# Performance work log

Hardware: AMD Instinct MI355X
Metric: run time of the kernel (lower is better)

Reference implementation:

```python
import jax, jax.numpy as jnp
import numpy as np

EPS = 1e-5

def _layer_norm_last(x):
    # F.layer_norm over the last dim, no affine
    m = jnp.mean(x, axis=-1, keepdims=True)
    v = jnp.var(x, axis=-1, keepdims=True)
    return (x - m) * jax.lax.rsqrt(v + EPS)

def setup_inputs() -> dict:
    key = jax.random.key(0)
    ks = jax.random.split(key, 4)
    N, C, H, W = 8, 512, 32, 32
    G = 8
    x = jax.random.normal(ks[0], (N, C, H, W), dtype=jnp.float32)
    w_qkv = jax.random.normal(ks[1], (3 * C, C), dtype=jnp.float32) * 0.02
    relative = jax.random.normal(ks[2], (3, 2 * C - 1), dtype=jnp.float32)
    bn_w = jnp.ones((3 * G,), dtype=jnp.float32)
    bn_b = jnp.zeros((3 * G,), dtype=jnp.float32)
    return {
        "x": x, "w_qkv": w_qkv, "relative": relative,
        "bn_w": bn_w, "bn_b": bn_b,
        "f_qr": jnp.float32(0.1), "f_kr": jnp.float32(0.1),
        "f_sv": jnp.float32(1.0), "f_sve": jnp.float32(0.1),
        "gamma": jnp.full((1,), 0.5, dtype=jnp.float32),
    }

def reference(x, w_qkv, relative, bn_w, bn_b, f_qr, f_kr, f_sv, f_sve, gamma):
    N, C, H, W = x.shape
    HW = H * W
    G = bn_w.shape[0] // 3          # groups
    gp = HW // G                    # group_planes

    # qkv transform (1x1 conv == matmul over channels) + layernorm over spatial
    x1 = x.reshape(N, C, HW)
    x1 = jnp.einsum('oc,bci->boi', w_qkv, x1)          # (N, 3C, HW)
    x1 = _layer_norm_last(x1)

    qkv = x1.reshape(N, G, 3 * C, gp)                  # row-major, matches torch
    q = qkv[:, :, :C]                                  # (N, G, C, gp)
    k = qkv[:, :, C:2 * C]
    v = qkv[:, :, 2 * C:]

    # relative position embeddings gathered to (3, C, C)
    qi = jnp.arange(C)[None, :]
    ki = jnp.arange(C)[:, None]
    rel_idx = (ki - qi + C - 1).reshape(-1)            # (C*C,) int
    emb = relative[:, rel_idx].reshape(3, C, C)
    qE, kE, vE = emb[0], emb[1], emb[2]

    # 'bgci,icj->bgcj' with emb repeated along i collapses to sum over i then outer
    qr = jnp.einsum('bgci,cj->bgcj', q, qE) * f_qr     # (N, G, C, C)
    kr = jnp.swapaxes(jnp.einsum('bgci,cj->bgcj', k, kE), 2, 3) * f_kr
    qk = jnp.einsum('bgci,bgji->bgcj', q, k)           # (N, G, C, C)

    ss = jnp.concatenate([qk, qr, kr], axis=1)         # (N, 3G, C, C)
    # BatchNorm2d (training mode: batch stats over N, C, C axes)
    mu = jnp.mean(ss, axis=(0, 2, 3), keepdims=True)
    var = jnp.var(ss, axis=(0, 2, 3), keepdims=True)
    ss = (ss - mu) * jax.lax.rsqrt(var + EPS)
    ss = ss * bn_w.reshape(1, -1, 1, 1) + bn_b.reshape(1, -1, 1, 1)

    ss = ss.reshape(N, 3, G, C, C).sum(axis=1)         # (N, G, C, C)
    sim = jax.nn.softmax(ss, axis=3)

    sv = jnp.einsum('bgci,bgij->bgjc', sim, v) * f_sv  # (N, G, gp, C)
    # 'bgci,jci->bgjc' with vE repeated along j -> same value for every j
    sve = jnp.einsum('bgci,ci->bgc', sim, vE) * f_sve  # (N, G, C)
    sve = jnp.broadcast_to(sve[:, :, None, :], sv.shape)

    so = jnp.concatenate([sv, sve], axis=-1).reshape(N, HW * 2, C)
    so = jnp.swapaxes(_layer_norm_last(jnp.swapaxes(so, 1, 2)), 1, 2)
    out = so.reshape(N, G, gp, 2, C).sum(axis=-2).reshape(N, C, H, W)
    return gamma.reshape(()) * out + x
```

## Files before the change

### kernel.cpp

```cpp
#include <hip/hip_runtime.h>
#include <math.h>

#define DEV_INLINE __device__ __forceinline__

typedef short bf16x8 __attribute__((ext_vector_type(8)));
typedef float f32x4  __attribute__((ext_vector_type(4)));


DEV_INLINE float bf2f(short h){
  union { unsigned u; float f; } x; x.u = ((unsigned)(unsigned short)h) << 16; return x.f;
}
DEV_INLINE short f2bf(float f){
  union { float f; unsigned u; } x; x.f = f;
  unsigned r = x.u + 0x7FFF + ((x.u >> 16) & 1);
  return (short)(r >> 16);
}

template<bool MAXOP>
DEV_INLINE float block_reduce_f(float v){
  __shared__ float tmp[4];
  const int lane = threadIdx.x & 63, w = threadIdx.x >> 6;
  #pragma unroll
  for (int off = 32; off; off >>= 1){
    float o = __shfl_down(v, off);
    v = MAXOP ? fmaxf(v, o) : (v + o);
  }
  __syncthreads();
  if (lane == 0) tmp[w] = v;
  __syncthreads();
  return MAXOP ? fmaxf(fmaxf(tmp[0], tmp[1]), fmaxf(tmp[2], tmp[3]))
               : (tmp[0] + tmp[1] + tmp[2] + tmp[3]);
}

DEV_INLINE double block_reduce_d(double v){
  __shared__ double tmp[4];
  const int lane = threadIdx.x & 63, w = threadIdx.x >> 6;
  #pragma unroll
  for (int off = 32; off; off >>= 1) v += __shfl_down(v, off);
  __syncthreads();
  if (lane == 0) tmp[w] = v;
  __syncthreads();
  return tmp[0] + tmp[1] + tmp[2] + tmp[3];
}


DEV_INLINE void stage_tile(const short* __restrict__ g, int ldk, char* lds_region, int t){
  #pragma unroll
  for (int r = 0; r < 2; ++r){
    int o   = t * 16 + r * 4096;
    int row = o >> 6, wb = o & 63;
    int swb = wb ^ (((row >> 1) & 3) << 4);
    const short* src = g + (size_t)row * ldk + (swb >> 1);
    char* dst = lds_region + ((t >> 6) << 10) + (r << 12);
    __builtin_amdgcn_global_load_lds((const __attribute__((address_space(1))) void*)src,
                                     (__attribute__((address_space(3))) void*)dst, 16, 0, 0);
  }
}

DEV_INLINE bf16x8 read_frag(const char* base, int row, int kgrp){
  int off = row * 64 + ((kgrp ^ ((row >> 1) & 3)) << 4);
  return *(const bf16x8*)(base + off);
}

template<int KTILES>
DEV_INLINE void mfma_loop(const short* __restrict__ A, int ldA,
                          const short* __restrict__ B, int ldB,
                          char* ldsA, char* ldsB, int t, f32x4 acc[4][4]){
  const int l = t & 63, w = t >> 6;
  const int wr = (w >> 1) * 64, wc = (w & 1) * 64;
  for (int kt = 0; kt < KTILES; ++kt){
    stage_tile(A + kt * 32, ldA, ldsA, t);
    stage_tile(B + kt * 32, ldB, ldsB, t);
    __syncthreads();
    bf16x8 af[4], bfr[4];
    #pragma unroll
    for (int m = 0; m < 4; ++m) af[m]  = read_frag(ldsA, wr + m * 16 + (l & 15), l >> 4);
    #pragma unroll
    for (int n = 0; n < 4; ++n) bfr[n] = read_frag(ldsB, wc + n * 16 + (l & 15), l >> 4);
    #pragma unroll
    for (int m = 0; m < 4; ++m)
      #pragma unroll
      for (int n = 0; n < 4; ++n)
        acc[m][n] = __builtin_amdgcn_mfma_f32_16x16x32_bf16(af[m], bfr[n], acc[m][n], 0, 0, 0);
    __syncthreads();
  }
}

__global__ __launch_bounds__(256) void k_prep(const float* __restrict__ X, short* __restrict__ Xt,
                                              const float* __restrict__ W, short* __restrict__ Wbf,
                                              double* __restrict__ stats, float* __restrict__ S12){
  __shared__ short s[64][72];
  const int bid = blockIdx.x;
  const int t = threadIdx.x;
  if (bid < 1024){
    const int it = bid & 15, kt = (bid >> 4) & 7, b = bid >> 7;
    const int rl = t >> 2, cs = (t & 3) * 16;
    const float* src = X + ((size_t)b * 512 + kt * 64 + rl) * 1024 + it * 64 + cs;
    #pragma unroll
    for (int e = 0; e < 16; e += 4){
      float4 v = *(const float4*)(src + e);
      s[rl][cs + e + 0] = f2bf(v.x); s[rl][cs + e + 1] = f2bf(v.y);
      s[rl][cs + e + 2] = f2bf(v.z); s[rl][cs + e + 3] = f2bf(v.w);
    }
    __syncthreads();
    bf16x8 a0, a1;
    #pragma unroll
    for (int e = 0; e < 8; ++e){ a0[e] = s[cs + e][rl]; a1[e] = s[cs + 8 + e][rl]; }
    short* dst = Xt + ((size_t)b * 1024 + it * 64 + rl) * 512 + kt * 64 + cs;
    *(bf16x8*)dst = a0;
    *(bf16x8*)(dst + 8) = a1;
  } else {
    const int gi = (bid - 1024) * 256 + t;
    if (gi < 48) stats[gi] = 0.0;
    if (gi < 8192) S12[gi] = 0.f;
    const int i = gi * 4;
    float4 v = *(const float4*)(W + i);
    short4 o; o.x = f2bf(v.x); o.y = f2bf(v.y); o.z = f2bf(v.z); o.w = f2bf(v.w);
    *(short4*)(Wbf + i) = o;
  }
}

__global__ __launch_bounds__(256) void k_vt(const short* __restrict__ Ybf, short* __restrict__ Vt){
  const int bg = blockIdx.z, iit = blockIdx.y, jt = blockIdx.x;
  const int b = bg >> 3, g = bg & 7;
  const short* V = Ybf + (size_t)(b * 1536 + g * 192 + 128) * 1024;
  __shared__ short s[64][72];
  const int t = threadIdx.x;
  const int rl = t >> 2, cs = (t & 3) * 16;
  const short* src = V + (size_t)(iit * 64 + rl) * 128 + jt * 64 + cs;
  *(bf16x8*)&s[rl][cs]     = *(const bf16x8*)src;
  *(bf16x8*)&s[rl][cs + 8] = *(const bf16x8*)(src + 8);
  __syncthreads();
  bf16x8 a0, a1;
  #pragma unroll
  for (int e = 0; e < 8; ++e){ a0[e] = s[cs + e][rl]; a1[e] = s[cs + 8 + e][rl]; }
  short* dst = Vt + ((size_t)bg * 128 + jt * 64 + rl) * 512 + iit * 64 + cs;
  *(bf16x8*)dst = a0;
  *(bf16x8*)(dst + 8) = a1;
}

__global__ __launch_bounds__(256) void k_gemm1(const short* __restrict__ Wbf,
                                               const short* __restrict__ Xt,
                                               short* __restrict__ Ybf){
  const int b = blockIdx.z, mt = blockIdx.y, nt = blockIdx.x;
  __shared__ char lds[16384];
  const int t = threadIdx.x;
  f32x4 acc[4][4];
  #pragma unroll
  for (int m = 0; m < 4; ++m)
    #pragma unroll
    for (int n = 0; n < 4; ++n) acc[m][n] = {0.f, 0.f, 0.f, 0.f};
  const short* A = Wbf + (size_t)mt * 128 * 512;
  const short* B = Xt + (size_t)b * 1024 * 512 + (size_t)nt * 128 * 512;
  mfma_loop<16>(A, 512, B, 512, lds, lds + 8192, t, acc);
  const int l = t & 63, w = t >> 6, wr = (w >> 1) * 64, wc = (w & 1) * 64;
  short* out = Ybf + (size_t)b * 1536 * 1024 + (size_t)(mt * 128 + wr) * 1024 + nt * 128 + wc;
  #pragma unroll
  for (int m = 0; m < 4; ++m)
    #pragma unroll
    for (int n = 0; n < 4; ++n)
      #pragma unroll
      for (int j = 0; j < 4; ++j)
        out[(size_t)(m * 16 + (l >> 4) * 4 + j) * 1024 + n * 16 + (l & 15)] = f2bf(acc[m][n][j]);
}

__global__ __launch_bounds__(256) void k_ln(short* __restrict__ Ybf,
                                            float* __restrict__ QS, float* __restrict__ KS){
  const int row = blockIdx.x * 4 + (threadIdx.x >> 6);
  const int l = threadIdx.x & 63;
  short* p = Ybf + (size_t)row * 1024 + l * 16;
  bf16x8 v0 = *(const bf16x8*)p;
  bf16x8 v1 = *(const bf16x8*)(p + 8);
  float f[16];
  #pragma unroll
  for (int e = 0; e < 8; ++e){ f[e] = bf2f(v0[e]); f[8 + e] = bf2f(v1[e]); }
  float s1 = 0.f, s2 = 0.f;
  #pragma unroll
  for (int e = 0; e < 16; ++e){ s1 += f[e]; s2 += f[e] * f[e]; }
  #pragma unroll
  for (int off = 32; off; off >>= 1){ s1 += __shfl_xor(s1, off); s2 += __shfl_xor(s2, off); }
  float mean = s1 * (1.f / 1024.f);
  float r = rsqrtf(s2 * (1.f / 1024.f) - mean * mean + 1e-5f);
  float cs = 0.f;
  #pragma unroll
  for (int e = 0; e < 16; ++e){ f[e] = (f[e] - mean) * r; cs += f[e]; }
  bf16x8 o0, o1;
  #pragma unroll
  for (int e = 0; e < 8; ++e){ o0[e] = f2bf(f[e]); o1[e] = f2bf(f[8 + e]); }
  *(bf16x8*)p = o0;
  *(bf16x8*)(p + 8) = o1;
  cs += __shfl_xor(cs, 1); cs += __shfl_xor(cs, 2); cs += __shfl_xor(cs, 4);
  const int o = row % 1536, ol = o % 192;
  if ((l & 7) == 0 && ol < 128){
    const int b = row / 1536, g = o / 192;
    const int c = (ol & 63) * 8 + (l >> 3);
    const int idx = (b * 8 + g) * 512 + c;
    if (ol < 64) QS[idx] = cs; else KS[idx] = cs;
  }
}

__global__ __launch_bounds__(256) void k_qk(const short* __restrict__ Ybf,
                                            short* __restrict__ QKbf,
                                            double* __restrict__ stats){
  const int bg = blockIdx.z, mt = blockIdx.y, nt = blockIdx.x;
  const int b = bg >> 3, g = bg & 7;
  __shared__ char lds[16384];
  const int t = threadIdx.x;
  f32x4 acc[4][4];
  #pragma unroll
  for (int m = 0; m < 4; ++m)
    #pragma unroll
    for (int n = 0; n < 4; ++n) acc[m][n] = {0.f, 0.f, 0.f, 0.f};
  const short* q  = Ybf + (size_t)(b * 1536 + g * 192) * 1024;
  const short* kp = q + 65536;
  mfma_loop<4>(q + (size_t)mt * 128 * 128, 128, kp + (size_t)nt * 128 * 128, 128,
               lds, lds + 8192, t, acc);
  const int l = t & 63, w = t >> 6, wr = (w >> 1) * 64, wc = (w & 1) * 64;
  short* out = QKbf + (size_t)bg * 512 * 512 + (size_t)(mt * 128 + wr) * 512 + nt * 128 + wc;
  float s1 = 0.f, s2 = 0.f;
  #pragma unroll
  for (int m = 0; m < 4; ++m)
    #pragma unroll
    for (int n = 0; n < 4; ++n)
      #pragma unroll
      for (int j = 0; j < 4; ++j){
        float vl = acc[m][n][j];
        s1 += vl; s2 += vl * vl;
        out[(size_t)(m * 16 + (l >> 4) * 4 + j) * 512 + n * 16 + (l & 15)] = f2bf(vl);
      }
  float S1 = block_reduce_f<false>(s1);
  float S2 = block_reduce_f<false>(s2);
  if (t == 0){
    atomicAdd(&stats[g * 6 + 0], (double)S1);
    atomicAdd(&stats[g * 6 + 1], (double)S2);
  }
}

__global__ __launch_bounds__(256) void k_qrkr(const float* __restrict__ QS,
                                              const float* __restrict__ KS,
                                              const float* __restrict__ rel,
                                              double* __restrict__ stats){
  const int g = blockIdx.x & 7, ch = blockIdx.x >> 3;
  const int t = threadIdx.x;
  const int c = ch * 64 + (t >> 2), part = t & 3;
  float r1 = 0, r2 = 0, r3 = 0, r4 = 0;
  for (int d = part * 128; d < part * 128 + 128; ++d){
    float v0 = rel[c + d];        r1 += v0; r2 += v0 * v0;
    float v1 = rel[1023 + c + d]; r3 += v1; r4 += v1 * v1;
  }
  #pragma unroll
  for (int off = 1; off < 4; off <<= 1){
    r1 += __shfl_xor(r1, off); r2 += __shfl_xor(r2, off);
    r3 += __shfl_xor(r3, off); r4 += __shfl_xor(r4, off);
  }
  double sq1 = 0, sq2 = 0, sk1 = 0, sk2 = 0;
  if (part == 0){
    float qa = 0, qb = 0, ka = 0, kb = 0;
    for (int b = 0; b < 8; ++b){
      float v = QS[(size_t)(b * 8 + g) * 512 + c]; qa += v; qb += v * v;
      float w = KS[(size_t)(b * 8 + g) * 512 + c]; ka += w; kb += w * w;
    }
    sq1 = (double)r1 * qa; sq2 = (double)r2 * qb;
    sk1 = (double)r3 * ka; sk2 = (double)r4 * kb;
  }
  sq1 = block_reduce_d(sq1);
  sq2 = block_reduce_d(sq2);
  sk1 = block_reduce_d(sk1);
  sk2 = block_reduce_d(sk2);
  if (t == 0){
    atomicAdd(&stats[g * 6 + 2], sq1);
    atomicAdd(&stats[g * 6 + 3], sq2);
    atomicAdd(&stats[g * 6 + 4], sk1);
    atomicAdd(&stats[g * 6 + 5], sk2);
  }
}

__global__ __launch_bounds__(256) void k_softmax(short* __restrict__ QKbf,
    const float* __restrict__ QS, const float* __restrict__ KS,
    const float* __restrict__ rel, const double* __restrict__ stats,
    const float* __restrict__ bnw, const float* __restrict__ bnb,
    const float* __restrict__ fqr, const float* __restrict__ fkr,
    const float* __restrict__ fsve, float* __restrict__ SVE, float* __restrict__ S12){
  const int row = blockIdx.x * 4 + (threadIdx.x >> 6);
  const int l = threadIdx.x & 63;
  const int bg = row >> 9, c = row & 511, g = bg & 7;
  const double M = 2097152.0;
  double mu0  = stats[g*6+0] / M;
  double var0 = stats[g*6+1] / M - mu0*mu0;
  double A0d  = (double)bnw[g] / sqrt(var0 + 1e-5);
  double fq   = (double)fqr[0];
  double mu1  = fq * stats[g*6+2] / M;
  double var1 = fq*fq * stats[g*6+3] / M - mu1*mu1;
  double A1d  = (double)bnw[8+g] / sqrt(var1 + 1e-5);
  double fk   = (double)fkr[0];
  double mu2  = fk * stats[g*6+4] / M;
  double var2 = fk*fk * stats[g*6+5] / M - mu2*mu2;
  double A2d  = (double)bnw[16+g] / sqrt(var2 + 1e-5);
  double Cgd  = ((double)bnb[g] - mu0*A0d) + ((double)bnb[8+g] - mu1*A1d)
              + ((double)bnb[16+g] - mu2*A2d);
  const float A0 = (float)A0d, B2 = (float)(A2d * fk), Cg = (float)Cgd;
  const float B1q = (float)(A1d * fq) * QS[row];

  short* __restrict__ qkrow = QKbf + (size_t)row * 512;
  const float* __restrict__ ksrow = KS + (size_t)bg * 512;
  const int j0 = l * 8;
  bf16x8 qk8 = *(const bf16x8*)(qkrow + j0);
  float4 ks0 = *(const float4*)(ksrow + j0);
  float4 ks1 = *(const float4*)(ksrow + j0 + 4);
  float ks[8] = {ks0.x, ks0.y, ks0.z, ks0.w, ks1.x, ks1.y, ks1.z, ks1.w};
  const float* relq = rel + 511 + c - j0;
  const float* relk = rel + 1534 + j0 - c;
  float s[8];
  float m = -1e30f;
  #pragma unroll
  for (int e = 0; e < 8; ++e){
    s[e] = A0 * bf2f(qk8[e]) + B1q * relq[-e] + B2 * ks[e] * relk[e] + Cg;
    m = fmaxf(m, s[e]);
  }
  #pragma unroll
  for (int off = 32; off; off >>= 1) m = fmaxf(m, __shfl_xor(m, off));
  float sum = 0.f;
  #pragma unroll
  for (int e = 0; e < 8; ++e){ s[e] = __expf(s[e] - m); sum += s[e]; }
  #pragma unroll
  for (int off = 32; off; off >>= 1) sum += __shfl_xor(sum, off);
  const float inv = 1.0f / sum;
  const float* relv = rel + 2557 + c - j0;
  float sve = 0.f;
  bf16x8 p8;
  #pragma unroll
  for (int e = 0; e < 8; ++e){
    float p = s[e] * inv;
    p8[e] = f2bf(p);
    sve += p * relv[-e];
  }
  *(bf16x8*)(qkrow + j0) = p8;
  #pragma unroll
  for (int off = 32; off; off >>= 1) sve += __shfl_xor(sve, off);
  if (l == 0){
    float e = fsve[0] * sve;
    SVE[row] = e;
    const int b = bg >> 3;
    atomicAdd(&S12[b * 512 + c],        128.f * e);
    atomicAdd(&S12[4096 + b * 512 + c], 128.f * e * e);
  }
}

__global__ __launch_bounds__(256) void k_sv(const short* __restrict__ Pbf,
                                            const short* __restrict__ Vt,
                                            const float* __restrict__ fsv,
                                            short* __restrict__ SV2,
                                            float* __restrict__ S12){
  const int bg = blockIdx.z, mt = blockIdx.x;
  __shared__ char lds[16384];
  __shared__ float s1buf[128], s2buf[128];
  const int t = threadIdx.x;
  s1buf[t & 127] = 0.f; s2buf[t & 127] = 0.f;
  f32x4 acc[4][4];
  #pragma unroll
  for (int m = 0; m < 4; ++m)
    #pragma unroll
    for (int n = 0; n < 4; ++n) acc[m][n] = {0.f, 0.f, 0.f, 0.f};
  const short* A = Pbf + (size_t)bg * 512 * 512 + (size_t)mt * 128 * 512;
  const short* B = Vt  + (size_t)bg * 128 * 512;
  mfma_loop<16>(A, 512, B, 512, lds, lds + 8192, t, acc);
  const int l = t & 63, w = t >> 6, wr = (w >> 1) * 64, wc = (w & 1) * 64;
  const float fv = fsv[0];
  short* out = SV2 + (size_t)bg * 512 * 128 + (size_t)(mt * 128 + wr) * 128 + wc;
  #pragma unroll
  for (int m = 0; m < 4; ++m)
    #pragma unroll
    for (int jr = 0; jr < 4; ++jr){
      float p1 = 0.f, p2 = 0.f;
      #pragma unroll
      for (int n = 0; n < 4; ++n){
        float vl = acc[m][n][jr] * fv;
        p1 += vl; p2 += vl * vl;
        out[(size_t)(m * 16 + (l >> 4) * 4 + jr) * 128 + n * 16 + (l & 15)] = f2bf(vl);
      }
      #pragma unroll
      for (int off = 1; off < 16; off <<= 1){
        p1 += __shfl_xor(p1, off);
        p2 += __shfl_xor(p2, off);
      }
      if ((l & 15) == 0){
        int rloc = wr + m * 16 + (l >> 4) * 4 + jr;
        atomicAdd(&s1buf[rloc], p1);
        atomicAdd(&s2buf[rloc], p2);
      }
    }
  __syncthreads();
  if (t < 128){
    const int b = bg >> 3;
    const int ci = b * 512 + mt * 128 + t;
    atomicAdd(&S12[ci],        s1buf[t]);
    atomicAdd(&S12[4096 + ci], s2buf[t]);
  }
}

__global__ __launch_bounds__(256) void k_out(const short* __restrict__ SV2,
    const float* __restrict__ SVE, const float* __restrict__ S12,
    const float* __restrict__ X, const float* __restrict__ gam, float* __restrict__ OUT){
  const int c2t = blockIdx.x, g = blockIdx.y, b = blockIdx.z;
  const int bg = b * 8 + g;
  const int c20 = c2t * 64;
  __shared__ float s[64][129];
  const int t = threadIdx.x;
  {
    const int col8 = (t & 15) * 8;
    #pragma unroll
    for (int r0 = 0; r0 < 64; r0 += 16){
      int row = r0 + (t >> 4);
      bf16x8 v = *(const bf16x8*)(SV2 + (size_t)bg * 65536 + (size_t)(c20 + row) * 128 + col8);
      #pragma unroll
      for (int e = 0; e < 8; ++e) s[row][col8 + e] = bf2f(v[e]);
    }
  }
  __syncthreads();
  const int lane = t & 63, w = t >> 6;
  const int c2 = c20 + lane;
  const float sm1 = S12[b * 512 + c2];
  const float sm2 = S12[4096 + b * 512 + c2];
  const float mean = sm1 * (1.f / 2048.f);
  const float rs   = rsqrtf(sm2 * (1.f / 2048.f) - mean * mean + 1e-5f);
  const float e    = SVE[(size_t)bg * 512 + c2];
  const float gm   = gam[0];
  for (int j = w; j < 128; j += 4){
    float v = s[lane][j];
    float o = (v + e - 2.f * mean) * rs;
    int chan = g * 64 + (j >> 1);
    size_t oi = ((size_t)b * 512 + chan) * 1024 + ((j & 1) << 9) + c2;
    OUT[oi] = gm * o + X[oi];
  }
}

extern "C" void kernel_launch(void* const* d_in, const int* in_sizes, int n_in,
                              void* d_out, int out_size, void* d_ws, size_t ws_size,
                              hipStream_t stream){
  const float* X    = (const float*)d_in[0];
  const float* W    = (const float*)d_in[1];
  const float* REL  = (const float*)d_in[2];
  const float* BNW  = (const float*)d_in[3];
  const float* BNB  = (const float*)d_in[4];
  const float* FQR  = (const float*)d_in[5];
  const float* FKR  = (const float*)d_in[6];
  const float* FSV  = (const float*)d_in[7];
  const float* FSVE = (const float*)d_in[8];
  const float* GAM  = (const float*)d_in[9];
  float* OUT = (float*)d_out;

  char* ws = (char*)d_ws;
  short*  Ybf   = (short*) (ws + 0ull);
  short*  QKbf  = (short*) (ws + 25165824ull);
  short*  SV2   = (short*) (ws + 58720256ull);
  short*  Wbf   = (short*) (ws + 75497472ull);
  short*  Xt    = (short*) (ws + 77070336ull);
  short*  Vt    = (short*) (ws + 85458944ull);
  float*  QS    = (float*) (ws + 93847552ull);
  float*  KS    = (float*) (ws + 93978624ull);
  float*  SVE   = (float*) (ws + 94109696ull);
  double* STATS = (double*)(ws + 94240768ull);
  float*  S12   = (float*) (ws + 94249472ull);

  k_prep   <<<1792,            256, 0, stream>>>(X, Xt, W, Wbf, STATS, S12);
  k_gemm1  <<<dim3(8, 12, 8),  256, 0, stream>>>(Wbf, Xt, Ybf);
  k_ln     <<<3072,            256, 0, stream>>>(Ybf, QS, KS);
  k_qk     <<<dim3(4, 4, 64),  256, 0, stream>>>(Ybf, QKbf, STATS);
  k_qrkr   <<<64,              256, 0, stream>>>(QS, KS, REL, STATS);
  k_vt     <<<dim3(2, 8, 64),  256, 0, stream>>>(Ybf, Vt);
  k_softmax<<<8192,            256, 0, stream>>>(QKbf, QS, KS, REL, STATS,
                                                 BNW, BNB, FQR, FKR, FSVE, SVE, S12);
  k_sv     <<<dim3(4, 1, 64),  256, 0, stream>>>(QKbf, Vt, FSV, SV2, S12);
  k_out    <<<dim3(8, 8, 8),   256, 0, stream>>>(SV2, SVE, S12, X, GAM, OUT);
}
```

Measured before the change: 131.4 us.

## Load MFMA fragments directly from global, split SV tiles, drop softmax max pass

```diff
diff --git a/kernel.cpp b/kernel.cpp
--- a/kernel.cpp
+++ b/kernel.cpp
@@ -42,7 +42,6 @@
   __syncthreads();
   return tmp[0] + tmp[1] + tmp[2] + tmp[3];
 }
-
 
 DEV_INLINE void stage_tile(const short* __restrict__ g, int ldk, char* lds_region, int t){
   #pragma unroll
@@ -204,19 +203,33 @@
                                             double* __restrict__ stats){
   const int bg = blockIdx.z, mt = blockIdx.y, nt = blockIdx.x;
   const int b = bg >> 3, g = bg & 7;
-  __shared__ char lds[16384];
-  const int t = threadIdx.x;
+  const int t = threadIdx.x, l = t & 63, w = t >> 6;
+  const int wr = (w >> 1) * 64, wc = (w & 1) * 64;
+  const short* __restrict__ q  = Ybf + (size_t)(b * 1536 + g * 192) * 1024 + (size_t)mt * 16384;
+  const short* __restrict__ kp = Ybf + (size_t)(b * 1536 + g * 192) * 1024 + 65536 + (size_t)nt * 16384;
   f32x4 acc[4][4];
   #pragma unroll
   for (int m = 0; m < 4; ++m)
     #pragma unroll
     for (int n = 0; n < 4; ++n) acc[m][n] = {0.f, 0.f, 0.f, 0.f};
-  const short* q  = Ybf + (size_t)(b * 1536 + g * 192) * 1024;
-  const short* kp = q + 65536;
-  mfma_loop<4>(q + (size_t)mt * 128 * 128, 128, kp + (size_t)nt * 128 * 128, 128,
-               lds, lds + 8192, t, acc);
-  const int l = t & 63, w = t >> 6, wr = (w >> 1) * 64, wc = (w & 1) * 64;
-  short* out = QKbf + (size_t)bg * 512 * 512 + (size_t)(mt * 128 + wr) * 512 + nt * 128 + wc;
+  const int rA = wr + (l & 15), rB = wc + (l & 15);
+  const int co = (l >> 4) * 8;
+  #pragma unroll 1
+  for (int kk = 0; kk < 4; ++kk){
+    bf16x8 af[4], bfr[4];
+    #pragma unroll
+    for (int m = 0; m < 4; ++m)
+      af[m] = *(const bf16x8*)(q + (size_t)(rA + m * 16) * 128 + kk * 32 + co);
+    #pragma unroll
+    for (int n = 0; n < 4; ++n)
+      bfr[n] = *(const bf16x8*)(kp + (size_t)(rB + n * 16) * 128 + kk * 32 + co);
+    #pragma unroll
+    for (int m = 0; m < 4; ++m)
+      #pragma unroll
+      for (int n = 0; n < 4; ++n)
+        acc[m][n] = __builtin_amdgcn_mfma_f32_16x16x32_bf16(af[m], bfr[n], acc[m][n], 0, 0, 0);
+  }
+  short* out = QKbf + (size_t)bg * 262144 + (size_t)(mt * 128 + wr) * 512 + nt * 128 + wc;
   float s1 = 0.f, s2 = 0.f;
   #pragma unroll
   for (int m = 0; m < 4; ++m)
@@ -311,17 +324,13 @@
   const float* relq = rel + 511 + c - j0;
   const float* relk = rel + 1534 + j0 - c;
   float s[8];
-  float m = -1e30f;
+  float sum = 0.f;
   #pragma unroll
   for (int e = 0; e < 8; ++e){
-    s[e] = A0 * bf2f(qk8[e]) + B1q * relq[-e] + B2 * ks[e] * relk[e] + Cg;
-    m = fmaxf(m, s[e]);
-  }
-  #pragma unroll
-  for (int off = 32; off; off >>= 1) m = fmaxf(m, __shfl_xor(m, off));
-  float sum = 0.f;
-  #pragma unroll
-  for (int e = 0; e < 8; ++e){ s[e] = __expf(s[e] - m); sum += s[e]; }
+    float sc = A0 * bf2f(qk8[e]) + B1q * relq[-e] + B2 * ks[e] * relk[e] + Cg;
+    s[e] = __expf(sc);
+    sum += s[e];
+  }
   #pragma unroll
   for (int off = 32; off; off >>= 1) sum += __shfl_xor(sum, off);
   const float inv = 1.0f / sum;
@@ -351,29 +360,45 @@
                                             const float* __restrict__ fsv,
                                             short* __restrict__ SV2,
                                             float* __restrict__ S12){
-  const int bg = blockIdx.z, mt = blockIdx.x;
-  __shared__ char lds[16384];
+  const int nt = blockIdx.x, mt = blockIdx.y, bg = blockIdx.z;
+  const int t = threadIdx.x, l = t & 63, w = t >> 6;
+  const int wr = (w >> 1) * 64, wc = (w & 1) * 32;
+  const short* __restrict__ A = Pbf + (size_t)bg * 262144 + (size_t)mt * 128 * 512;
+  const short* __restrict__ B = Vt  + (size_t)bg * 65536  + (size_t)nt * 64 * 512;
+  f32x4 acc[4][2];
+  #pragma unroll
+  for (int m = 0; m < 4; ++m)
+    #pragma unroll
+    for (int n = 0; n < 2; ++n) acc[m][n] = {0.f, 0.f, 0.f, 0.f};
+  const int rA = wr + (l & 15), rB = wc + (l & 15);
+  const int co = (l >> 4) * 8;
+  #pragma unroll 1
+  for (int kk = 0; kk < 16; ++kk){
+    bf16x8 af[4], bfr[2];
+    #pragma unroll
+    for (int m = 0; m < 4; ++m)
+      af[m] = *(const bf16x8*)(A + (size_t)(rA + m * 16) * 512 + kk * 32 + co);
+    #pragma unroll
+    for (int n = 0; n < 2; ++n)
+      bfr[n] = *(const bf16x8*)(B + (size_t)(rB + n * 16) * 512 + kk * 32 + co);
+    #pragma unroll
+    for (int m = 0; m < 4; ++m)
+      #pragma unroll
+      for (int n = 0; n < 2; ++n)
+        acc[m][n] = __builtin_amdgcn_mfma_f32_16x16x32_bf16(af[m], bfr[n], acc[m][n], 0, 0, 0);
+  }
   __shared__ float s1buf[128], s2buf[128];
-  const int t = threadIdx.x;
-  s1buf[t & 127] = 0.f; s2buf[t & 127] = 0.f;
-  f32x4 acc[4][4];
-  #pragma unroll
-  for (int m = 0; m < 4; ++m)
-    #pragma unroll
-    for (int n = 0; n < 4; ++n) acc[m][n] = {0.f, 0.f, 0.f, 0.f};
-  const short* A = Pbf + (size_t)bg * 512 * 512 + (size_t)mt * 128 * 512;
-  const short* B = Vt  + (size_t)bg * 128 * 512;
-  mfma_loop<16>(A, 512, B, 512, lds, lds + 8192, t, acc);
-  const int l = t & 63, w = t >> 6, wr = (w >> 1) * 64, wc = (w & 1) * 64;
+  if (t < 128){ s1buf[t] = 0.f; s2buf[t] = 0.f; }
+  __syncthreads();
   const float fv = fsv[0];
-  short* out = SV2 + (size_t)bg * 512 * 128 + (size_t)(mt * 128 + wr) * 128 + wc;
+  short* out = SV2 + (size_t)bg * 65536 + (size_t)(mt * 128 + wr) * 128 + nt * 64 + wc;
   #pragma unroll
   for (int m = 0; m < 4; ++m)
     #pragma unroll
     for (int jr = 0; jr < 4; ++jr){
       float p1 = 0.f, p2 = 0.f;
       #pragma unroll
-      for (int n = 0; n < 4; ++n){
+      for (int n = 0; n < 2; ++n){
         float vl = acc[m][n][jr] * fv;
         p1 += vl; p2 += vl * vl;
         out[(size_t)(m * 16 + (l >> 4) * 4 + jr) * 128 + n * 16 + (l & 15)] = f2bf(vl);
@@ -470,6 +495,6 @@
   k_vt     <<<dim3(2, 8, 64),  256, 0, stream>>>(Ybf, Vt);
   k_softmax<<<8192,            256, 0, stream>>>(QKbf, QS, KS, REL, STATS,
                                                  BNW, BNB, FQR, FKR, FSVE, SVE, S12);
-  k_sv     <<<dim3(4, 1, 64),  256, 0, stream>>>(QKbf, Vt, FSV, SV2, S12);
+  k_sv     <<<dim3(2, 4, 64),  256, 0, stream>>>(QKbf, Vt, FSV, SV2, S12);
   k_out    <<<dim3(8, 8, 8),   256, 0, stream>>>(SV2, SVE, S12, X, GAM, OUT);
 }
```

New measurement: 151.2 us. +15.1%, slower.
